# Kernel tuning notes

Measured on AMD Instinct MI355X. Metric: run time of the kernel, lower is better.

The kernel has to match this reference:

```python
import jax, jax.numpy as jnp
import numpy as np
from jax import lax

EPS = 1e-5
SLOPE = 0.2  # LeakyReLU negative slope
DN = ('NCHW', 'OIHW', 'NCHW')


def lrelu(x):
    return jnp.where(x > 0, x, SLOPE * x)


def bnorm(x, gb):
    # training-mode batchnorm over (N,H,W), biased variance (torch semantics)
    g, b = gb
    m = x.mean((0, 2, 3), keepdims=True)
    v = x.var((0, 2, 3), keepdims=True)
    return (x - m) * lax.rsqrt(v + EPS) * g.reshape(1, -1, 1, 1) + b.reshape(1, -1, 1, 1)


def conv_down(x, w):
    # Conv2d(k=4, s=2, p=1, bias=False)
    return lax.conv_general_dilated(x, w, (2, 2), ((1, 1), (1, 1)), dimension_numbers=DN)


def conv_up(x, w):
    # ConvTranspose2d(k=4, s=2, p=1, bias=False); w in torch layout [in, out, kh, kw]
    wt = jnp.flip(w, (2, 3)).transpose(1, 0, 2, 3)  # -> OIHW
    return lax.conv_general_dilated(x, wt, (1, 1), ((2, 2), (2, 2)), lhs_dilation=(2, 2), dimension_numbers=DN)


def setup_inputs() -> dict:
    key = jax.random.key(0)
    ks = jax.random.split(key, 16)
    N, B = 256, 8
    S = 0.05  # weight init scale

    def w(k, shape, s=S):
        return jax.random.normal(k, shape, jnp.float32) * s

    def bn_p(c):
        return (jnp.ones((c,), jnp.float32), jnp.zeros((c,), jnp.float32))

    return {
        'x': jax.random.normal(ks[0], (B, 3, N, N), jnp.float32),
        'w_d1': w(ks[1], (32, 3, 4, 4)),
        'w_d2': w(ks[2], (128, 32, 4, 4)), 'bn_d2': bn_p(128),
        'w_d3': w(ks[3], (256, 128, 4, 4)), 'bn_d3': bn_p(256),
        'w_d4': w(ks[4], (256, 256, 4, 4)), 'bn_d4': bn_p(256),
        'w_d5': w(ks[5], (256, 256, 4, 4)),
        'w_u1': w(ks[6], (256, 256, 4, 4)), 'bn_u1': bn_p(256),
        'w_u2': w(ks[7], (512, 256, 4, 4)), 'bn_u2': bn_p(256),
        'w_u3': w(ks[8], (512, 128, 4, 4)), 'bn_u3': bn_p(128),
        'w_u4': w(ks[9], (256, 32, 4, 4)), 'bn_u4': bn_p(32),
        'w_fin': w(ks[10], (3, 64, 4, 4)),
        'b_fin': jnp.zeros((3,), jnp.float32),
        'Wr': w(ks[11], (N, N), 1.0 / 16.0),
        'Wi': w(ks[12], (N, N), 1.0 / 16.0),
    }


def reference(x, w_d1, w_d2, bn_d2, w_d3, bn_d3, w_d4, bn_d4, w_d5,
              w_u1, bn_u1, w_u2, bn_u2, w_u3, bn_u3, w_u4, bn_u4,
              w_fin, b_fin, Wr, Wi):
    # ---- UNet encoder ----
    d1 = lrelu(conv_down(x, w_d1))                 # [B,32,128,128]
    d2 = lrelu(bnorm(conv_down(d1, w_d2), bn_d2))  # [B,128,64,64]
    d3 = lrelu(bnorm(conv_down(d2, w_d3), bn_d3))  # [B,256,32,32]
    d4 = lrelu(bnorm(conv_down(d3, w_d4), bn_d4))  # [B,256,16,16]
    d5 = lrelu(conv_down(d4, w_d5))                # [B,256,8,8]

    # ---- UNet decoder ----
    def up(xin, wt, gb, skip):
        y = jax.nn.relu(bnorm(conv_up(xin, wt), gb))
        return jnp.concatenate([y, skip], axis=1)

    u1 = up(d5, w_u1, bn_u1, d4)   # [B,512,16,16]
    u2 = up(u1, w_u2, bn_u2, d3)   # [B,512,32,32]
    u3 = up(u2, w_u3, bn_u3, d2)   # [B,256,64,64]
    u45 = up(u3, w_u4, bn_u4, d1)  # [B,64,128,128]

    # ---- final: nearest upsample x2, ZeroPad2d((1,0,1,0)), conv k4 p1, tanh ----
    y = jnp.repeat(jnp.repeat(u45, 2, axis=2), 2, axis=3)          # [B,64,256,256]
    y = jnp.pad(y, ((0, 0), (0, 0), (1, 0), (1, 0)))               # pad top/left by 1
    y = lax.conv_general_dilated(y, w_fin, (1, 1), ((1, 1), (1, 1)), dimension_numbers=DN)
    u_out = jnp.tanh(y + b_fin.reshape(1, -1, 1, 1))               # [B,3,256,256]

    # ---- hand-rolled 2D 'DFT' as batched complex matmuls ----
    # rows: fft_in_rows = u_out @ W^T where W = Wr + i*Wi (nn.Linear is x @ W^T)
    Rr = jnp.einsum('bchw,nw->bchn', u_out, Wr)
    Ri = jnp.einsum('bchw,nw->bchn', u_out, Wi)
    # cols: fft_in_cols[:,k] = fft_in_rows[:,k] @ W  =>  fft_in_cols = W^T @ fft_in_rows
    Cr = jnp.einsum('hm,bchn->bcmn', Wr, Rr) - jnp.einsum('hm,bchn->bcmn', Wi, Ri)
    Ci = jnp.einsum('hm,bchn->bcmn', Wr, Ri) + jnp.einsum('hm,bchn->bcmn', Wi, Rr)
    res = jnp.concatenate([Cr, Ci], axis=-1)  # [B,3,N,2N]
    return (u_out, res)
```

## Files before the change

### kernel.cpp

```cpp
#include <hip/hip_runtime.h>
#include <math.h>

#define LRELU_SLOPE 0.2f
#define BN_EPS 1e-5f

#define WROW(COB8) ((COB8) * 20 + ((COB8) >> 3) * 4)
#define WIDX(cc, col, COB8) ((cc) * WROW(COB8) + (col) * 20 + ((col) >> 3) * 4)

template<int PX>
__global__ __launch_bounds__(256) void conv_down_t(
    const float* __restrict__ in, const float* __restrict__ w,
    float* __restrict__ out,
    int Cin, int CinW, int IH, int IW, int Cout, int OH, int OW,
    int inCt, int inCoff, int outCt, int outCoff,
    int PGB, int CICH, int act, int CS, size_t pstride)
{
    constexpr int NC = 2 * PX + 2;
    extern __shared__ float wl[];
    const int nthr = blockDim.x;
    const int COB8 = (nthr / PGB) * 8;
    const int tid = threadIdx.x;
    const int pg  = tid % PGB;
    const int cog = tid / PGB;
    const int s   = blockIdx.z % CS;
    const int b   = blockIdx.z / CS;
    const int ciBase = s * Cin;
    out += (size_t)s * pstride;
    const int co_base = blockIdx.y * COB8;

    const int gid = blockIdx.x * PGB + pg;
    const int px0 = gid * PX;
    const int oy = px0 / OW, ox0 = px0 - oy * OW;
    const int iy0 = 2 * oy - 1, ix0 = 2 * ox0 - 1;
    const bool interior = (iy0 >= 0) && (iy0 + 3 < IH) && (ix0 >= 0) && (ix0 + NC - 1 < IW);

    float acc[8][PX];
#pragma unroll
    for (int j = 0; j < 8; ++j)
#pragma unroll
        for (int p = 0; p < PX; ++p) acc[j][p] = 0.f;

    const float* ibase = in + ((size_t)b * inCt + inCoff + ciBase) * IH * IW;

    for (int ci0 = 0; ci0 < Cin; ci0 += CICH) {
        __syncthreads();
        const int nel = CICH * COB8 * 16;
        for (int idx = tid; idx < nel; idx += nthr) {
            const int t = idx & 15;
            const int rest = idx >> 4;
            const int col = rest % COB8;
            const int cc  = rest / COB8;
            wl[WIDX(cc, col, COB8) + t] =
                w[((size_t)(co_base + col) * CinW + ciBase + ci0 + cc) * 16 + t];
        }
        __syncthreads();

        for (int cc = 0; cc < CICH; ++cc) {
            const float* q = ibase + (size_t)(ci0 + cc) * IH * IW;
            const float* wc = wl + WIDX(cc, cog * 8, COB8);
#pragma unroll
            for (int ky = 0; ky < 4; ++ky) {
                float v[NC];
                const int ry = iy0 + ky;
                if (interior) {
                    const float* r = q + ry * IW + ix0;
#pragma unroll
                    for (int c = 0; c < NC; ++c) v[c] = r[c];
                } else {
                    const bool vy = (unsigned)ry < (unsigned)IH;
                    const float* r = q + (vy ? ry : 0) * IW;
#pragma unroll
                    for (int c = 0; c < NC; ++c) {
                        const int cx = ix0 + c;
                        const bool ok = vy && ((unsigned)cx < (unsigned)IW);
                        v[c] = ok ? r[cx] : 0.f;
                    }
                }
#pragma unroll
                for (int j = 0; j < 8; ++j) {
                    const float4 wk = *(const float4*)(wc + j * 20 + ky * 4);
#pragma unroll
                    for (int p = 0; p < PX; ++p) {
                        acc[j][p] = fmaf(v[2 * p + 0], wk.x, acc[j][p]);
                        acc[j][p] = fmaf(v[2 * p + 1], wk.y, acc[j][p]);
                        acc[j][p] = fmaf(v[2 * p + 2], wk.z, acc[j][p]);
                        acc[j][p] = fmaf(v[2 * p + 3], wk.w, acc[j][p]);
                    }
                }
            }
        }
    }

    const size_t chs = (size_t)OH * OW;
    float* ob = out + ((size_t)b * outCt + outCoff + co_base + cog * 8) * chs + px0;
#pragma unroll
    for (int j = 0; j < 8; ++j) {
#pragma unroll
        for (int p = 0; p < PX; ++p) {
            float y = acc[j][p];
            if (act == 1) y = y > 0.f ? y : LRELU_SLOPE * y;
            acc[j][p] = y;
        }
        if constexpr (PX == 4) {
            *(float4*)(ob + j * chs) = make_float4(acc[j][0], acc[j][1], acc[j][2], acc[j][3]);
        } else if constexpr (PX == 2) {
            *(float2*)(ob + j * chs) = make_float2(acc[j][0], acc[j][1]);
        } else {
            ob[j * chs] = acc[j][0];
        }
    }
}

template<int PX>
__global__ __launch_bounds__(256) void conv_up_t(
    const float* __restrict__ in, const float* __restrict__ w,
    float* __restrict__ out,
    int Cin, int IH, int IW, int Cout, int OH, int OW,
    int inCt, int inCoff, int outCt, int outCoff,
    int PGB, int CICH, int CS, size_t pstride)
{
    constexpr int NC = (PX >> 1) + 2;
    extern __shared__ float wl[];
    const int nthr = blockDim.x;
    const int COB8 = (nthr / PGB) * 8;
    const int tid = threadIdx.x;
    const int pg  = tid % PGB;
    const int cog = tid / PGB;
    const int s   = blockIdx.z % CS;
    const int b   = blockIdx.z / CS;
    const int ciBase = s * Cin;
    out += (size_t)s * pstride;
    const int co_base = blockIdx.y * COB8;

    const int gid = blockIdx.x * PGB + pg;
    const int px0 = gid * PX;
    const int oy = px0 / OW, ox0 = px0 - oy * OW;
    const int kya = (oy + 1) & 1, kyb = kya + 2;
    const int iya = (oy + 1) >> 1, iyb = iya - 1;
    const int cb = ((ox0 + 1) >> 1) - 1;
    const bool interior = (iyb >= 0) && (iya < IH) && (cb >= 0) && (cb + NC - 1 < IW);

    float acc[8][PX];
#pragma unroll
    for (int j = 0; j < 8; ++j)
#pragma unroll
        for (int p = 0; p < PX; ++p) acc[j][p] = 0.f;

    const float* ibase = in + ((size_t)b * inCt + inCoff + ciBase) * IH * IW;

    for (int ci0 = 0; ci0 < Cin; ci0 += CICH) {
        __syncthreads();
        const int nel = CICH * COB8 * 16;
        for (int idx = tid; idx < nel; idx += nthr) {
            const int t = idx & 15;
            const int rest = idx >> 4;
            const int col = rest % COB8;
            const int cc  = rest / COB8;
            wl[WIDX(cc, col, COB8) + t] =
                w[((size_t)(ciBase + ci0 + cc) * Cout + co_base + col) * 16 + t];
        }
        __syncthreads();

        for (int cc = 0; cc < CICH; ++cc) {
            const float* q = ibase + (size_t)(ci0 + cc) * IH * IW;
            const float* wc = wl + WIDX(cc, cog * 8, COB8);
            float va[NC], vb[NC];
            if (interior) {
                const float* ra = q + iya * IW + cb;
                const float* rb = q + iyb * IW + cb;
#pragma unroll
                for (int c = 0; c < NC; ++c) { va[c] = ra[c]; vb[c] = rb[c]; }
            } else {
                const bool vya = iya < IH, vyb = iyb >= 0;
                const float* ra = q + (vya ? iya : 0) * IW;
                const float* rb = q + (vyb ? iyb : 0) * IW;
#pragma unroll
                for (int c = 0; c < NC; ++c) {
                    const int cx = cb + c;
                    const bool okc = (unsigned)cx < (unsigned)IW;
                    va[c] = (vya && okc) ? ra[cx] : 0.f;
                    vb[c] = (vyb && okc) ? rb[cx] : 0.f;
                }
            }
#pragma unroll
            for (int j = 0; j < 8; ++j) {
                const float4 wA4 = *(const float4*)(wc + j * 20 + kya * 4);
                const float4 wB4 = *(const float4*)(wc + j * 20 + kyb * 4);
                const float wA[4] = {wA4.x, wA4.y, wA4.z, wA4.w};
                const float wB[4] = {wB4.x, wB4.y, wB4.z, wB4.w};
#pragma unroll
                for (int p = 0; p < PX; ++p) {
                    const int la = ((p + 1) >> 1) + 1, lb = la - 1;
                    const int ka = (p + 1) & 1, kb = ka + 2;
                    acc[j][p] = fmaf(va[la], wA[ka], acc[j][p]);
                    acc[j][p] = fmaf(va[lb], wA[kb], acc[j][p]);
                    acc[j][p] = fmaf(vb[la], wB[ka], acc[j][p]);
                    acc[j][p] = fmaf(vb[lb], wB[kb], acc[j][p]);
                }
            }
        }
    }

    const size_t chs = (size_t)OH * OW;
    float* ob = out + ((size_t)b * outCt + outCoff + co_base + cog * 8) * chs + px0;
#pragma unroll
    for (int j = 0; j < 8; ++j) {
        if constexpr (PX == 4) {
            *(float4*)(ob + j * chs) = make_float4(acc[j][0], acc[j][1], acc[j][2], acc[j][3]);
        } else if constexpr (PX == 2) {
            *(float2*)(ob + j * chs) = make_float2(acc[j][0], acc[j][1]);
        } else {
            ob[j * chs] = acc[j][0];
        }
    }
}

__global__ __launch_bounds__(256) void bn_stats_k(
    const float* __restrict__ in, float* __restrict__ mean, float* __restrict__ var,
    int B, int C, int HW, int NS, size_t pstride)
{
    const int c = blockIdx.x;
    const int tid = threadIdx.x;
    const int n = B * HW;
    double s = 0.0, s2 = 0.0;
    for (int e = tid; e < n; e += 256) {
        const int b = e / HW, pix = e - b * HW;
        const size_t idx = ((size_t)(b * C + c)) * HW + pix;
        float v = in[idx];
        for (int p = 1; p < NS; ++p) v += in[(size_t)p * pstride + idx];
        s += v; s2 += (double)v * v;
    }
    __shared__ double sh[256], sh2[256];
    sh[tid] = s; sh2[tid] = s2;
    __syncthreads();
    for (int st = 128; st > 0; st >>= 1) {
        if (tid < st) { sh[tid] += sh[tid + st]; sh2[tid] += sh2[tid + st]; }
        __syncthreads();
    }
    if (tid == 0) {
        const double m = sh[0] / n;
        mean[c] = (float)m;
        var[c] = (float)(sh2[0] / n - m * m);
    }
}

__global__ __launch_bounds__(256) void bn_act_k(
    const float* __restrict__ in, const float* __restrict__ mean,
    const float* __restrict__ var, const float* __restrict__ g,
    const float* __restrict__ beta, float* __restrict__ out,
    int B, int C, int HW, int act, int Ct, int coff, int NS, size_t pstride)
{
    const size_t n = (size_t)B * C * HW;
    for (size_t i = (size_t)blockIdx.x * 256 + threadIdx.x; i < n; i += (size_t)gridDim.x * 256) {
        const int pix = (int)(i % HW);
        const int c = (int)((i / HW) % C);
        const int b = (int)(i / ((size_t)HW * C));
        float x = in[i];
        for (int p = 1; p < NS; ++p) x += in[(size_t)p * pstride + i];
        float y = (x - mean[c]) * rsqrtf(var[c] + BN_EPS) * g[c] + beta[c];
        if (act == 1) y = y > 0.f ? y : LRELU_SLOPE * y;
        else if (act == 2) y = fmaxf(y, 0.f);
        out[((size_t)(b * Ct + coff + c)) * HW + pix] = y;
    }
}

__global__ __launch_bounds__(256) void combine_act_k(
    const float* __restrict__ in, float* __restrict__ out,
    size_t n, int NS, size_t pstride, int act)
{
    for (size_t i = (size_t)blockIdx.x * 256 + threadIdx.x; i < n; i += (size_t)gridDim.x * 256) {
        float v = in[i];
        for (int p = 1; p < NS; ++p) v += in[(size_t)p * pstride + i];
        if (act == 1) v = v > 0.f ? v : LRELU_SLOPE * v;
        out[i] = v;
    }
}

__global__ __launch_bounds__(256) void final_k(
    const float* __restrict__ u, const float* __restrict__ w,
    const float* __restrict__ bias, float* __restrict__ out, int B)
{
    __shared__ float wl[3 * 64 * 16];
    const int b = blockIdx.z;
    const int tid = threadIdx.x;
    for (int i = tid; i < 3 * 64 * 16; i += 256) wl[i] = w[i];
    __syncthreads();

    const int opix = blockIdx.x * 256 + tid;
    const int oy = opix >> 8, ox = opix & 255;
    const float* ib = u + (size_t)b * 64 * 128 * 128;
    float acc[3] = {bias[0], bias[1], bias[2]};

    int o[16];
    bool ok[16];
    const int r0 = (oy - 2) >> 1, r1 = (oy - 1) >> 1, r2 = oy >> 1, r3 = (oy + 1) >> 1;
    const int c0 = (ox - 2) >> 1, c1 = (ox - 1) >> 1, c2 = ox >> 1, c3 = (ox + 1) >> 1;
    const int rr[4] = {r0, r1, r2, r3};
    const int cc4[4] = {c0, c1, c2, c3};
    const bool interior = (oy >= 2 && oy <= 254 && ox >= 2 && ox <= 254);
#pragma unroll
    for (int ky = 0; ky < 4; ++ky)
#pragma unroll
        for (int kx = 0; kx < 4; ++kx) {
            const int h = oy - 2 + ky, xx = ox - 2 + kx;
            const bool v = ((unsigned)h < 256u) && ((unsigned)xx < 256u);
            ok[ky * 4 + kx] = v;
            const int rrr = v ? rr[ky] : 0, ccc = v ? cc4[kx] : 0;
            o[ky * 4 + kx] = rrr * 128 + ccc;
        }

    for (int ci = 0; ci < 64; ++ci) {
        const float* p = ib + ci * 16384;
        float v[16];
        if (interior) {
#pragma unroll
            for (int k = 0; k < 16; ++k) v[k] = p[o[k]];
        } else {
#pragma unroll
            for (int k = 0; k < 16; ++k) v[k] = ok[k] ? p[o[k]] : 0.f;
        }
#pragma unroll
        for (int co = 0; co < 3; ++co) {
            const float* wj = wl + (co * 64 + ci) * 16;
            const float4 w0 = *(const float4*)(wj + 0);
            const float4 w1 = *(const float4*)(wj + 4);
            const float4 w2 = *(const float4*)(wj + 8);
            const float4 w3 = *(const float4*)(wj + 12);
            acc[co] = fmaf(v[0], w0.x, acc[co]);  acc[co] = fmaf(v[1], w0.y, acc[co]);
            acc[co] = fmaf(v[2], w0.z, acc[co]);  acc[co] = fmaf(v[3], w0.w, acc[co]);
            acc[co] = fmaf(v[4], w1.x, acc[co]);  acc[co] = fmaf(v[5], w1.y, acc[co]);
            acc[co] = fmaf(v[6], w1.z, acc[co]);  acc[co] = fmaf(v[7], w1.w, acc[co]);
            acc[co] = fmaf(v[8], w2.x, acc[co]);  acc[co] = fmaf(v[9], w2.y, acc[co]);
            acc[co] = fmaf(v[10], w2.z, acc[co]); acc[co] = fmaf(v[11], w2.w, acc[co]);
            acc[co] = fmaf(v[12], w3.x, acc[co]); acc[co] = fmaf(v[13], w3.y, acc[co]);
            acc[co] = fmaf(v[14], w3.z, acc[co]); acc[co] = fmaf(v[15], w3.w, acc[co]);
        }
    }
#pragma unroll
    for (int co = 0; co < 3; ++co)
        out[((size_t)(b * 3 + co) * 256 + oy) * 256 + ox] = tanhf(acc[co]);
}

__global__ __launch_bounds__(256) void dft_rows_k(
    const float* __restrict__ U, const float* __restrict__ Wr,
    const float* __restrict__ Wi, float* __restrict__ Rr, float* __restrict__ Ri)
{
    __shared__ float Ut[16][17], Wrt[16][17], Wit[16][17];
    const int tx = threadIdx.x, ty = threadIdx.y;
    const int r = blockIdx.y * 16 + ty;
    const int nb = blockIdx.x * 16;
    float sr = 0.f, si = 0.f;
    for (int kk = 0; kk < 256; kk += 16) {
        Ut[ty][tx]  = U[(size_t)r * 256 + kk + tx];
        Wrt[ty][tx] = Wr[(size_t)(nb + ty) * 256 + kk + tx];
        Wit[ty][tx] = Wi[(size_t)(nb + ty) * 256 + kk + tx];
        __syncthreads();
#pragma unroll
        for (int t = 0; t < 16; ++t) {
            const float uv = Ut[ty][t];
            sr = fmaf(uv, Wrt[tx][t], sr);
            si = fmaf(uv, Wit[tx][t], si);
        }
        __syncthreads();
    }
    Rr[(size_t)r * 256 + nb + tx] = sr;
    Ri[(size_t)r * 256 + nb + tx] = si;
}

__global__ __launch_bounds__(256) void dft_cols_k(
    const float* __restrict__ Wr, const float* __restrict__ Wi,
    const float* __restrict__ Rr, const float* __restrict__ Ri,
    float* __restrict__ res)
{
    __shared__ float Wrt[16][17], Wit[16][17], Rrt[16][17], Rit[16][17];
    const int tx = threadIdx.x, ty = threadIdx.y;
    const int bc = blockIdx.z;
    const int mb = blockIdx.y * 16, nb = blockIdx.x * 16;
    float cr = 0.f, ci = 0.f;
    for (int hh = 0; hh < 256; hh += 16) {
        Wrt[ty][tx] = Wr[(size_t)(hh + ty) * 256 + mb + tx];
        Wit[ty][tx] = Wi[(size_t)(hh + ty) * 256 + mb + tx];
        Rrt[ty][tx] = Rr[((size_t)bc * 256 + hh + ty) * 256 + nb + tx];
        Rit[ty][tx] = Ri[((size_t)bc * 256 + hh + ty) * 256 + nb + tx];
        __syncthreads();
#pragma unroll
        for (int t = 0; t < 16; ++t) {
            const float wr = Wrt[t][ty], wi = Wit[t][ty];
            const float rr = Rrt[t][tx], ri = Rit[t][tx];
            cr = fmaf(wr, rr, cr);  cr = fmaf(-wi, ri, cr);
            ci = fmaf(wr, ri, ci);  ci = fmaf(wi, rr, ci);
        }
        __syncthreads();
    }
    const int m = mb + ty, n = nb + tx;
    res[((size_t)bc * 256 + m) * 512 + n] = cr;
    res[((size_t)bc * 256 + m) * 512 + 256 + n] = ci;
}

static inline void take_bn(void* const* d_in, const int* in_sizes, int& i, int C,
                           const float*& g, const float*& b)
{
    if (in_sizes[i] == C) {
        g = (const float*)d_in[i];
        b = (const float*)d_in[i + 1];
        i += 2;
    } else {
        g = (const float*)d_in[i];
        b = g + C;
        i += 1;
    }
}

static inline int nblk(size_t n) { return (int)((n + 255) / 256); }
static inline size_t lds_bytes(int cich, int cob8) {
    return (size_t)cich * WROW(cob8) * 4;
}
static inline int pick_cs(int want, size_t out_elems, size_t tmp_cap) {
    int cs = want;
    while (cs > 1 && out_elems * (size_t)cs > tmp_cap) cs >>= 1;
    return cs;
}
static inline int min_i(int a, int b) { return a < b ? a : b; }

extern "C" void kernel_launch(void* const* d_in, const int* in_sizes, int n_in,
                              void* d_out, int out_size, void* d_ws, size_t ws_size,
                              hipStream_t stream)
{
    const int B = 8;
    int i = 0;
    const float* x     = (const float*)d_in[i++];
    const float* w_d1  = (const float*)d_in[i++];
    const float* w_d2  = (const float*)d_in[i++];
    const float *g_d2, *b_d2; take_bn(d_in, in_sizes, i, 128, g_d2, b_d2);
    const float* w_d3  = (const float*)d_in[i++];
    const float *g_d3, *b_d3; take_bn(d_in, in_sizes, i, 256, g_d3, b_d3);
    const float* w_d4  = (const float*)d_in[i++];
    const float *g_d4, *b_d4; take_bn(d_in, in_sizes, i, 256, g_d4, b_d4);
    const float* w_d5  = (const float*)d_in[i++];
    const float* w_u1  = (const float*)d_in[i++];
    const float *g_u1, *b_u1; take_bn(d_in, in_sizes, i, 256, g_u1, b_u1);
    const float* w_u2  = (const float*)d_in[i++];
    const float *g_u2, *b_u2; take_bn(d_in, in_sizes, i, 256, g_u2, b_u2);
    const float* w_u3  = (const float*)d_in[i++];
    const float *g_u3, *b_u3; take_bn(d_in, in_sizes, i, 128, g_u3, b_u3);
    const float* w_u4  = (const float*)d_in[i++];
    const float *g_u4, *b_u4; take_bn(d_in, in_sizes, i, 32, g_u4, b_u4);
    const float* w_fin = (const float*)d_in[i++];
    const float* b_fin = (const float*)d_in[i++];
    const float* Wr    = (const float*)d_in[i++];
    const float* Wi    = (const float*)d_in[i++];

    float* ws = (float*)d_ws;
    size_t off = 0;
    float* u1b  = ws + off; off += (size_t)B * 512 * 16 * 16;
    float* u2b  = ws + off; off += (size_t)B * 512 * 32 * 32;
    float* u3b  = ws + off; off += (size_t)B * 256 * 64 * 64;
    float* u45b = ws + off; off += (size_t)B * 64 * 128 * 128;
    float* d5   = ws + off; off += (size_t)B * 256 * 8 * 8;
    float* bnm  = ws + off; off += 256;
    float* bnv  = ws + off; off += 256;
    float* tmp  = ws + off;
    size_t tmp_cap = (ws_size / 4 > off) ? (ws_size / 4 - off) : 0;
    if (tmp_cap < 4194304) tmp_cap = 4194304;
    if (tmp_cap > 8388608) tmp_cap = 8388608;

    float* Rr_buf = u3b;
    float* Ri_buf = u45b;

    float* u_out = (float*)d_out;
    float* res   = u_out + (size_t)B * 3 * 256 * 256;

    const size_t oe_d2 = (size_t)B * 128 * 4096;   const int cs_d2 = pick_cs(2, oe_d2, tmp_cap);
    const size_t oe_d3 = (size_t)B * 256 * 1024;   const int cs_d3 = pick_cs(4, oe_d3, tmp_cap);
    const size_t oe_d4 = (size_t)B * 256 * 256;    const int cs_d4 = pick_cs(8, oe_d4, tmp_cap);
    const size_t oe_d5 = (size_t)B * 256 * 64;     const int cs_d5 = pick_cs(8, oe_d5, tmp_cap);
    const size_t oe_u1 = (size_t)B * 256 * 256;    const int cs_u1 = pick_cs(8, oe_u1, tmp_cap);
    const size_t oe_u2 = (size_t)B * 256 * 1024;   const int cs_u2 = pick_cs(4, oe_u2, tmp_cap);
    const size_t oe_u3 = (size_t)B * 128 * 4096;   const int cs_u3 = pick_cs(2, oe_u3, tmp_cap);
    const size_t oe_u4 = (size_t)B * 32 * 16384;   const int cs_u4 = pick_cs(2, oe_u4, tmp_cap);

    conv_down_t<4><<<dim3(16, 4, B), 256, lds_bytes(3, 8), stream>>>(
        x, w_d1, u45b, 3, 3, 256, 256, 32, 128, 128, 3, 0, 64, 32, 256, 3, 1, 1, 0);
    {
        const int cin = 32 / cs_d2, cich = min_i(32, cin);
        conv_down_t<4><<<dim3(4, 16, B * cs_d2), 256, lds_bytes(cich, 8), stream>>>(
            u45b, w_d2, tmp, cin, 32, 128, 128, 128, 64, 64, 64, 32, 128, 0, 256, cich, 0, cs_d2, oe_d2);
        bn_stats_k<<<128, 256, 0, stream>>>(tmp, bnm, bnv, B, 128, 4096, cs_d2, oe_d2);
        bn_act_k<<<nblk(oe_d2), 256, 0, stream>>>(tmp, bnm, bnv, g_d2, b_d2, u3b, B, 128, 4096, 1, 256, 128, cs_d2, oe_d2);
    }
    {
        const int cin = 128 / cs_d3, cich = min_i(32, cin);
        conv_down_t<4><<<dim3(1, 32, B * cs_d3), 256, lds_bytes(cich, 8), stream>>>(
            u3b, w_d3, tmp, cin, 128, 64, 64, 256, 32, 32, 256, 128, 256, 0, 256, cich, 0, cs_d3, oe_d3);
        bn_stats_k<<<256, 256, 0, stream>>>(tmp, bnm, bnv, B, 256, 1024, cs_d3, oe_d3);
        bn_act_k<<<nblk(oe_d3), 256, 0, stream>>>(tmp, bnm, bnv, g_d3, b_d3, u2b, B, 256, 1024, 1, 512, 256, cs_d3, oe_d3);
    }
    {
        const int cin = 256 / cs_d4, cich = min_i(16, cin);
        conv_down_t<2><<<dim3(1, 16, B * cs_d4), 256, lds_bytes(cich, 16), stream>>>(
            u2b, w_d4, tmp, cin, 256, 32, 32, 256, 16, 16, 512, 256, 256, 0, 128, cich, 0, cs_d4, oe_d4);
        bn_stats_k<<<256, 256, 0, stream>>>(tmp, bnm, bnv, B, 256, 256, cs_d4, oe_d4);
        bn_act_k<<<nblk(oe_d4), 256, 0, stream>>>(tmp, bnm, bnv, g_d4, b_d4, u1b, B, 256, 256, 1, 512, 256, cs_d4, oe_d4);
    }
    {
        const int cin = 256 / cs_d5, cich = min_i(8, cin);
        conv_down_t<1><<<dim3(1, 8, B * cs_d5), 256, lds_bytes(cich, 32), stream>>>(
            u1b, w_d5, tmp, cin, 256, 16, 16, 256, 8, 8, 512, 256, 256, 0, 64, cich, 0, cs_d5, oe_d5);
        combine_act_k<<<nblk(oe_d5), 256, 0, stream>>>(tmp, d5, oe_d5, cs_d5, oe_d5, 1);
    }

    {
        const int cin = 256 / cs_u1, cich = min_i(16, cin);
        conv_up_t<2><<<dim3(1, 16, B * cs_u1), 256, lds_bytes(cich, 16), stream>>>(
            d5, w_u1, tmp, cin, 8, 8, 256, 16, 16, 256, 0, 256, 0, 128, cich, cs_u1, oe_u1);
        bn_stats_k<<<256, 256, 0, stream>>>(tmp, bnm, bnv, B, 256, 256, cs_u1, oe_u1);
        bn_act_k<<<nblk(oe_u1), 256, 0, stream>>>(tmp, bnm, bnv, g_u1, b_u1, u1b, B, 256, 256, 2, 512, 0, cs_u1, oe_u1);
    }
    {
        const int cin = 512 / cs_u2, cich = min_i(32, cin);
        conv_up_t<4><<<dim3(1, 32, B * cs_u2), 256, lds_bytes(cich, 8), stream>>>(
            u1b, w_u2, tmp, cin, 16, 16, 256, 32, 32, 512, 0, 256, 0, 256, cich, cs_u2, oe_u2);
        bn_stats_k<<<256, 256, 0, stream>>>(tmp, bnm, bnv, B, 256, 1024, cs_u2, oe_u2);
        bn_act_k<<<nblk(oe_u2), 256, 0, stream>>>(tmp, bnm, bnv, g_u2, b_u2, u2b, B, 256, 1024, 2, 512, 0, cs_u2, oe_u2);
    }
    {
        const int cin = 512 / cs_u3, cich = min_i(32, cin);
        conv_up_t<4><<<dim3(4, 16, B * cs_u3), 256, lds_bytes(cich, 8), stream>>>(
            u2b, w_u3, tmp, cin, 32, 32, 128, 64, 64, 512, 0, 128, 0, 256, cich, cs_u3, oe_u3);
        bn_stats_k<<<128, 256, 0, stream>>>(tmp, bnm, bnv, B, 128, 4096, cs_u3, oe_u3);
        bn_act_k<<<nblk(oe_u3), 256, 0, stream>>>(tmp, bnm, bnv, g_u3, b_u3, u3b, B, 128, 4096, 2, 256, 0, cs_u3, oe_u3);
    }
    {
        const int cin = 256 / cs_u4, cich = min_i(32, cin);
        conv_up_t<4><<<dim3(16, 4, B * cs_u4), 256, lds_bytes(cich, 8), stream>>>(
            u3b, w_u4, tmp, cin, 64, 64, 32, 128, 128, 256, 0, 32, 0, 256, cich, cs_u4, oe_u4);
        bn_stats_k<<<32, 256, 0, stream>>>(tmp, bnm, bnv, B, 32, 16384, cs_u4, oe_u4);
        bn_act_k<<<nblk(oe_u4), 256, 0, stream>>>(tmp, bnm, bnv, g_u4, b_u4, u45b, B, 32, 16384, 2, 64, 0, cs_u4, oe_u4);
    }

    final_k<<<dim3(256, 1, B), 256, 0, stream>>>(u45b, w_fin, b_fin, u_out, B);

    dft_rows_k<<<dim3(16, 384), dim3(16, 16), 0, stream>>>(u_out, Wr, Wi, Rr_buf, Ri_buf);
    dft_cols_k<<<dim3(16, 16, 24), dim3(16, 16), 0, stream>>>(Wr, Wi, Rr_buf, Ri_buf, res);
}
```

Baseline: 2.164 ms.

## Split BN statistics into two-stage reduction and vectorize BN/act kernels

The batchnorm statistics kernel, which previously used one block per channel, is split into a chunked partial-sum kernel over a 2D grid plus a small wave-shuffle finalize kernel. This spreads the reduction across more blocks for better parallelism. The normalize/activation and combine kernels now use float4 loads and stores, and the normalize kernel uses one block per (batch, channel) row with a precomputed scale and shift, which removes the per-element div/mod indexing. The cost is one extra launch per BN layer, and the code now assumes HW is divisible by 4*NB.

```diff
diff --git a/kernel.cpp b/kernel.cpp
--- a/kernel.cpp
+++ b/kernel.cpp
@@ -215,20 +215,29 @@
     }
 }
 
-__global__ __launch_bounds__(256) void bn_stats_k(
-    const float* __restrict__ in, float* __restrict__ mean, float* __restrict__ var,
-    int B, int C, int HW, int NS, size_t pstride)
+__global__ __launch_bounds__(256) void bn_stats1_k(
+    const float* __restrict__ in, double* __restrict__ part,
+    int B, int C, int HW, int NS, size_t pstride, int NB)
 {
     const int c = blockIdx.x;
+    const int chunk = blockIdx.y;
     const int tid = threadIdx.x;
-    const int n = B * HW;
+    const int vper = (HW >> 2) / NB;
+    const int v0 = chunk * vper, v1 = v0 + vper;
     double s = 0.0, s2 = 0.0;
-    for (int e = tid; e < n; e += 256) {
-        const int b = e / HW, pix = e - b * HW;
-        const size_t idx = ((size_t)(b * C + c)) * HW + pix;
-        float v = in[idx];
-        for (int p = 1; p < NS; ++p) v += in[(size_t)p * pstride + idx];
-        s += v; s2 += (double)v * v;
+    for (int b = 0; b < B; ++b) {
+        const size_t rowv = (((size_t)b * C + c) * HW) >> 2;
+        const float4* p0 = (const float4*)in + rowv;
+        for (int v = v0 + tid; v < v1; v += 256) {
+            float4 a = p0[v];
+            for (int p = 1; p < NS; ++p) {
+                const float4* pp = (const float4*)(in + (size_t)p * pstride) + rowv;
+                const float4 t4 = pp[v];
+                a.x += t4.x; a.y += t4.y; a.z += t4.z; a.w += t4.w;
+            }
+            s += (double)a.x + a.y + a.z + a.w;
+            s2 += (double)a.x * a.x + (double)a.y * a.y + (double)a.z * a.z + (double)a.w * a.w;
+        }
     }
     __shared__ double sh[256], sh2[256];
     sh[tid] = s; sh2[tid] = s2;
@@ -238,9 +247,27 @@
         __syncthreads();
     }
     if (tid == 0) {
-        const double m = sh[0] / n;
+        part[(size_t)(c * NB + chunk) * 2 + 0] = sh[0];
+        part[(size_t)(c * NB + chunk) * 2 + 1] = sh2[0];
+    }
+}
+
+__global__ __launch_bounds__(64) void bn_stats2_k(
+    const double* __restrict__ part, float* __restrict__ mean,
+    float* __restrict__ var, int n, int NB)
+{
+    const int c = blockIdx.x;
+    const int t = threadIdx.x;
+    double s  = (t < NB) ? part[(size_t)(c * NB + t) * 2 + 0] : 0.0;
+    double s2 = (t < NB) ? part[(size_t)(c * NB + t) * 2 + 1] : 0.0;
+    for (int o = 32; o > 0; o >>= 1) {
+        s  += __shfl_down(s, o, 64);
+        s2 += __shfl_down(s2, o, 64);
+    }
+    if (t == 0) {
+        const double m = s / n;
         mean[c] = (float)m;
-        var[c] = (float)(sh2[0] / n - m * m);
+        var[c] = (float)(s2 / n - m * m);
     }
 }
 
@@ -248,31 +275,55 @@
     const float* __restrict__ in, const float* __restrict__ mean,
     const float* __restrict__ var, const float* __restrict__ g,
     const float* __restrict__ beta, float* __restrict__ out,
-    int B, int C, int HW, int act, int Ct, int coff, int NS, size_t pstride)
-{
-    const size_t n = (size_t)B * C * HW;
-    for (size_t i = (size_t)blockIdx.x * 256 + threadIdx.x; i < n; i += (size_t)gridDim.x * 256) {
-        const int pix = (int)(i % HW);
-        const int c = (int)((i / HW) % C);
-        const int b = (int)(i / ((size_t)HW * C));
-        float x = in[i];
-        for (int p = 1; p < NS; ++p) x += in[(size_t)p * pstride + i];
-        float y = (x - mean[c]) * rsqrtf(var[c] + BN_EPS) * g[c] + beta[c];
-        if (act == 1) y = y > 0.f ? y : LRELU_SLOPE * y;
-        else if (act == 2) y = fmaxf(y, 0.f);
-        out[((size_t)(b * Ct + coff + c)) * HW + pix] = y;
+    int C, int HW, int act, int Ct, int coff, int NS, size_t pstride)
+{
+    const int bc = blockIdx.x;
+    const int c = bc % C, b = bc / C;
+    const float sc = rsqrtf(var[c] + BN_EPS) * g[c];
+    const float sh = beta[c] - mean[c] * sc;
+    const size_t rowv = (((size_t)b * C + c) * HW) >> 2;
+    const float4* p0 = (const float4*)in + rowv;
+    float4* o4 = (float4*)(out + ((size_t)(b * Ct + coff + c)) * HW);
+    const int nv = HW >> 2;
+    for (int v = threadIdx.x; v < nv; v += 256) {
+        float4 a = p0[v];
+        for (int p = 1; p < NS; ++p) {
+            const float4* pp = (const float4*)(in + (size_t)p * pstride) + rowv;
+            const float4 t4 = pp[v];
+            a.x += t4.x; a.y += t4.y; a.z += t4.z; a.w += t4.w;
+        }
+        a.x = a.x * sc + sh; a.y = a.y * sc + sh;
+        a.z = a.z * sc + sh; a.w = a.w * sc + sh;
+        if (act == 1) {
+            a.x = a.x > 0.f ? a.x : LRELU_SLOPE * a.x;
+            a.y = a.y > 0.f ? a.y : LRELU_SLOPE * a.y;
+            a.z = a.z > 0.f ? a.z : LRELU_SLOPE * a.z;
+            a.w = a.w > 0.f ? a.w : LRELU_SLOPE * a.w;
+        } else if (act == 2) {
+            a.x = fmaxf(a.x, 0.f); a.y = fmaxf(a.y, 0.f);
+            a.z = fmaxf(a.z, 0.f); a.w = fmaxf(a.w, 0.f);
+        }
+        o4[v] = a;
     }
 }
 
 __global__ __launch_bounds__(256) void combine_act_k(
     const float* __restrict__ in, float* __restrict__ out,
-    size_t n, int NS, size_t pstride, int act)
-{
-    for (size_t i = (size_t)blockIdx.x * 256 + threadIdx.x; i < n; i += (size_t)gridDim.x * 256) {
-        float v = in[i];
-        for (int p = 1; p < NS; ++p) v += in[(size_t)p * pstride + i];
-        if (act == 1) v = v > 0.f ? v : LRELU_SLOPE * v;
-        out[i] = v;
+    size_t nv, int NS, size_t pstride, int act)
+{
+    for (size_t v = (size_t)blockIdx.x * 256 + threadIdx.x; v < nv; v += (size_t)gridDim.x * 256) {
+        float4 a = ((const float4*)in)[v];
+        for (int p = 1; p < NS; ++p) {
+            const float4 t4 = ((const float4*)(in + (size_t)p * pstride))[v];
+            a.x += t4.x; a.y += t4.y; a.z += t4.z; a.w += t4.w;
+        }
+        if (act == 1) {
+            a.x = a.x > 0.f ? a.x : LRELU_SLOPE * a.x;
+            a.y = a.y > 0.f ? a.y : LRELU_SLOPE * a.y;
+            a.z = a.z > 0.f ? a.z : LRELU_SLOPE * a.z;
+            a.w = a.w > 0.f ? a.w : LRELU_SLOPE * a.w;
+        }
+        ((float4*)out)[v] = a;
     }
 }
 
@@ -459,6 +510,7 @@
     float* d5   = ws + off; off += (size_t)B * 256 * 8 * 8;
     float* bnm  = ws + off; off += 256;
     float* bnv  = ws + off; off += 256;
+    double* part = (double*)(ws + off); off += 8192;
     float* tmp  = ws + off;
     size_t tmp_cap = (ws_size / 4 > off) ? (ws_size / 4 - off) : 0;
     if (tmp_cap < 4194304) tmp_cap = 4194304;
@@ -479,67 +531,67 @@
     const size_t oe_u3 = (size_t)B * 128 * 4096;   const int cs_u3 = pick_cs(2, oe_u3, tmp_cap);
     const size_t oe_u4 = (size_t)B * 32 * 16384;   const int cs_u4 = pick_cs(2, oe_u4, tmp_cap);
 
+    #define BN_LAYER(C_, HW_, NB_, g_, b_, dst_, act_, Ct_, coff_, cs_, oe_)                 \
+        bn_stats1_k<<<dim3(C_, NB_), 256, 0, stream>>>(tmp, part, B, C_, HW_, cs_, oe_, NB_);\
+        bn_stats2_k<<<C_, 64, 0, stream>>>(part, bnm, bnv, B * HW_, NB_);                    \
+        bn_act_k<<<B * C_, 256, 0, stream>>>(tmp, bnm, bnv, g_, b_, dst_, C_, HW_, act_, Ct_, coff_, cs_, oe_)
+
     conv_down_t<4><<<dim3(16, 4, B), 256, lds_bytes(3, 8), stream>>>(
         x, w_d1, u45b, 3, 3, 256, 256, 32, 128, 128, 3, 0, 64, 32, 256, 3, 1, 1, 0);
     {
         const int cin = 32 / cs_d2, cich = min_i(32, cin);
         conv_down_t<4><<<dim3(4, 16, B * cs_d2), 256, lds_bytes(cich, 8), stream>>>(
             u45b, w_d2, tmp, cin, 32, 128, 128, 128, 64, 64, 64, 32, 128, 0, 256, cich, 0, cs_d2, oe_d2);
-        bn_stats_k<<<128, 256, 0, stream>>>(tmp, bnm, bnv, B, 128, 4096, cs_d2, oe_d2);
-        bn_act_k<<<nblk(oe_d2), 256, 0, stream>>>(tmp, bnm, bnv, g_d2, b_d2, u3b, B, 128, 4096, 1, 256, 128, cs_d2, oe_d2);
+        BN_LAYER(128, 4096, 16, g_d2, b_d2, u3b, 1, 256, 128, cs_d2, oe_d2);
     }
     {
         const int cin = 128 / cs_d3, cich = min_i(32, cin);
         conv_down_t<4><<<dim3(1, 32, B * cs_d3), 256, lds_bytes(cich, 8), stream>>>(
             u3b, w_d3, tmp, cin, 128, 64, 64, 256, 32, 32, 256, 128, 256, 0, 256, cich, 0, cs_d3, oe_d3);
-        bn_stats_k<<<256, 256, 0, stream>>>(tmp, bnm, bnv, B, 256, 1024, cs_d3, oe_d3);
-        bn_act_k<<<nblk(oe_d3), 256, 0, stream>>>(tmp, bnm, bnv, g_d3, b_d3, u2b, B, 256, 1024, 1, 512, 256, cs_d3, oe_d3);
+        BN_LAYER(256, 1024, 8, g_d3, b_d3, u2b, 1, 512, 256, cs_d3, oe_d3);
     }
     {
         const int cin = 256 / cs_d4, cich = min_i(16, cin);
         conv_down_t<2><<<dim3(1, 16, B * cs_d4), 256, lds_bytes(cich, 16), stream>>>(
             u2b, w_d4, tmp, cin, 256, 32, 32, 256, 16, 16, 512, 256, 256, 0, 128, cich, 0, cs_d4, oe_d4);
-        bn_stats_k<<<256, 256, 0, stream>>>(tmp, bnm, bnv, B, 256, 256, cs_d4, oe_d4);
-        bn_act_k<<<nblk(oe_d4), 256, 0, stream>>>(tmp, bnm, bnv, g_d4, b_d4, u1b, B, 256, 256, 1, 512, 256, cs_d4, oe_d4);
+        BN_LAYER(256, 256, 8, g_d4, b_d4, u1b, 1, 512, 256, cs_d4, oe_d4);
     }
     {
         const int cin = 256 / cs_d5, cich = min_i(8, cin);
         conv_down_t<1><<<dim3(1, 8, B * cs_d5), 256, lds_bytes(cich, 32), stream>>>(
             u1b, w_d5, tmp, cin, 256, 16, 16, 256, 8, 8, 512, 256, 256, 0, 64, cich, 0, cs_d5, oe_d5);
-        combine_act_k<<<nblk(oe_d5), 256, 0, stream>>>(tmp, d5, oe_d5, cs_d5, oe_d5, 1);
+        combine_act_k<<<nblk(oe_d5 / 4), 256, 0, stream>>>(tmp, d5, oe_d5 / 4, cs_d5, oe_d5, 1);
     }
 
     {
         const int cin = 256 / cs_u1, cich = min_i(16, cin);
         conv_up_t<2><<<dim3(1, 16, B * cs_u1), 256, lds_bytes(cich, 16), stream>>>(
             d5, w_u1, tmp, cin, 8, 8, 256, 16, 16, 256, 0, 256, 0, 128, cich, cs_u1, oe_u1);
-        bn_stats_k<<<256, 256, 0, stream>>>(tmp, bnm, bnv, B, 256, 256, cs_u1, oe_u1);
-        bn_act_k<<<nblk(oe_u1), 256, 0, stream>>>(tmp, bnm, bnv, g_u1, b_u1, u1b, B, 256, 256, 2, 512, 0, cs_u1, oe_u1);
+        BN_LAYER(256, 256, 8, g_u1, b_u1, u1b, 2, 512, 0, cs_u1, oe_u1);
     }
     {
         const int cin = 512 / cs_u2, cich = min_i(32, cin);
         conv_up_t<4><<<dim3(1, 32, B * cs_u2), 256, lds_bytes(cich, 8), stream>>>(
             u1b, w_u2, tmp, cin, 16, 16, 256, 32, 32, 512, 0, 256, 0, 256, cich, cs_u2, oe_u2);
-        bn_stats_k<<<256, 256, 0, stream>>>(tmp, bnm, bnv, B, 256, 1024, cs_u2, oe_u2);
-        bn_act_k<<<nblk(oe_u2), 256, 0, stream>>>(tmp, bnm, bnv, g_u2, b_u2, u2b, B, 256, 1024, 2, 512, 0, cs_u2, oe_u2);
+        BN_LAYER(256, 1024, 8, g_u2, b_u2, u2b, 2, 512, 0, cs_u2, oe_u2);
     }
     {
         const int cin = 512 / cs_u3, cich = min_i(32, cin);
         conv_up_t<4><<<dim3(4, 16, B * cs_u3), 256, lds_bytes(cich, 8), stream>>>(
             u2b, w_u3, tmp, cin, 32, 32, 128, 64, 64, 512, 0, 128, 0, 256, cich, cs_u3, oe_u3);
-        bn_stats_k<<<128, 256, 0, stream>>>(tmp, bnm, bnv, B, 128, 4096, cs_u3, oe_u3);
-        bn_act_k<<<nblk(oe_u3), 256, 0, stream>>>(tmp, bnm, bnv, g_u3, b_u3, u3b, B, 128, 4096, 2, 256, 0, cs_u3, oe_u3);
+        BN_LAYER(128, 4096, 16, g_u3, b_u3, u3b, 2, 256, 0, cs_u3, oe_u3);
     }
     {
         const int cin = 256 / cs_u4, cich = min_i(32, cin);
         conv_up_t<4><<<dim3(16, 4, B * cs_u4), 256, lds_bytes(cich, 8), stream>>>(
             u3b, w_u4, tmp, cin, 64, 64, 32, 128, 128, 256, 0, 32, 0, 256, cich, cs_u4, oe_u4);
-        bn_stats_k<<<32, 256, 0, stream>>>(tmp, bnm, bnv, B, 32, 16384, cs_u4, oe_u4);
-        bn_act_k<<<nblk(oe_u4), 256, 0, stream>>>(tmp, bnm, bnv, g_u4, b_u4, u45b, B, 32, 16384, 2, 64, 0, cs_u4, oe_u4);
+        BN_LAYER(32, 16384, 64, g_u4, b_u4, u45b, 2, 64, 0, cs_u4, oe_u4);
     }
 
     final_k<<<dim3(256, 1, B), 256, 0, stream>>>(u45b, w_fin, b_fin, u_out, B);
 
     dft_rows_k<<<dim3(16, 384), dim3(16, 16), 0, stream>>>(u_out, Wr, Wi, Rr_buf, Ri_buf);
     dft_cols_k<<<dim3(16, 16, 24), dim3(16, 16), 0, stream>>>(Wr, Wi, Rr_buf, Ri_buf, res);
-}
+
+    #undef BN_LAYER
+}
```

New measurement: 1.840 ms. -15.0%, faster.
